# Kernel optimization log

Hardware: AMD Instinct MI355X
Metric: run time of the kernel (lower is better)

The kernel has to match this reference:

```python
import jax, jax.numpy as jnp
import numpy as np

MNIST_IM_SIZE = 784
LATENT = 128
BATCH_SIZE = 8192
ETA = 1.0
GAMMA = 1.0
EPS8 = 1e-8


def setup_inputs() -> dict:
    key = jax.random.key(0)
    ks = jax.random.split(key, 8)
    s = 0.02  # weight init scale
    H = MNIST_IM_SIZE * 4          # 3136
    D2 = MNIST_IM_SIZE // 2        # 392
    return {
        "x": jax.random.uniform(ks[0], (BATCH_SIZE, MNIST_IM_SIZE), jnp.float32),
        "eps": jax.random.normal(ks[1], (BATCH_SIZE, LATENT), jnp.float32),
        "W11": jax.random.normal(ks[2], (MNIST_IM_SIZE, H), jnp.float32) * s,
        "b11": jnp.zeros((H,), jnp.float32),
        "W31": jax.random.normal(ks[3], (H, LATENT), jnp.float32) * s,
        "b31": jnp.zeros((LATENT,), jnp.float32),
        "W32": jax.random.normal(ks[4], (H, LATENT), jnp.float32) * s,
        "b32": jnp.zeros((LATENT,), jnp.float32),
        "W44": jax.random.normal(ks[5], (LATENT, D2), jnp.float32) * s,
        "b44": jnp.zeros((D2,), jnp.float32),
        "W61": jax.random.normal(ks[6], (D2, MNIST_IM_SIZE), jnp.float32) * s,
        "b61": jnp.zeros((MNIST_IM_SIZE,), jnp.float32),
    }


def _clog(t):
    # torch BCELoss clamps log at -100
    return jnp.clip(jnp.log(t), -100.0)


def reference(x, eps, W11, b11, W31, b31, W32, b32, W44, b44, W61, b61):
    b2 = BATCH_SIZE // 2

    def encode(xi):
        enc = jax.nn.relu(xi @ W11 + b11)            # [b2, 4*IM]
        mu = jax.nn.relu(enc @ W31 + b31)            # [b2, LATENT]
        sigma = jax.nn.relu(enc @ W32 + b32)         # [b2, LATENT]
        return mu, sigma

    def decode(z):
        dec = jax.nn.relu(z @ W44 + b44)             # [b2, IM/2]
        dec = jax.nn.relu(dec @ W61 + b61)           # [b2, IM]
        return jax.nn.sigmoid(dec)

    x1, x2 = x[:b2], x[b2:]
    mu1, sig1 = encode(x1)
    mu2, sig2 = encode(x2)
    z1 = eps[:b2] * sig1 + mu1
    z2 = eps[b2:] * sig2 + mu2
    y = jnp.concatenate([decode(z1), decode(z2)], axis=0)  # [B, IM]

    # ---- MAE_loss ----
    sigma1 = sig1 + EPS8
    sigma2 = sig2 + EPS8
    rec_loss = -jnp.sum(x * _clog(y) + (1.0 - x) * _clog(1.0 - y))

    sig_m = (sigma1 + sigma2) * 0.5
    mu_m = (mu1 + mu2) * 0.5
    dkl_pq = 0.5 * jnp.sum(-1.0 - jnp.log(EPS8 + sig_m ** 2) + mu_m ** 2 + sig_m ** 2, axis=1)  # [b2]

    # Covariances are diagonal (as_strided diag copy) -> closed forms:
    # inv_cov = diag(1/sigma); det = prod(sigma); trace(inv_cov2 @ cov1) = sum(sigma1/sigma2)
    det1 = jnp.prod(sigma1, axis=1)                  # [b2]
    det2 = jnp.prod(sigma2, axis=1)                  # [b2]
    trace = jnp.sum(sigma1 / sigma2, axis=1)         # [b2]
    diff = mu2 - mu1
    dquad = jnp.sum(diff * diff / sigma2, axis=1)    # [b2]  (diff^T inv_cov2 diff)
    e = jnp.log(EPS8 + det2 / (det1 + EPS8)) - LATENT  # [b2]

    # torch broadcasting artifact: [b2,1,1]+[b2]+[b2] -> [b2,1,b2] -> resize(b2,b2)
    # => D[i,j] = 0.5*(dquad[i] + trace[j] + e[j])
    D = 0.5 * (dquad[:, None] + trace[None, :] + e[None, :])  # [b2, b2]

    l_diverse = jnp.sum(jnp.log1p(jnp.exp(-D)), axis=1)       # [b2]
    mean_qq = jnp.mean(D, axis=1)                             # [b2]
    # torch (b2,b2) - (b2,) broadcasts mean over the LAST axis (per column)
    l_smooth = jnp.sqrt(jnp.sum((D - mean_qq) ** 2, axis=1) / (LATENT - 1))

    loss = rec_loss + jnp.sum(dkl_pq) + ETA * jnp.sum(l_diverse) + GAMMA * jnp.sum(l_smooth)
    return y, loss
```

## Files before the change

kernel.cpp:

```cpp
#include <hip/hip_runtime.h>
#include <hip/hip_bf16.h>
#include <math.h>

#define BATCH   8192
#define IM      784
#define HDIM    3136
#define LAT     128
#define D2      392
#define B2      4096

#define IM_P    800
#define HDIM_P  3200
#define N2_P    256
#define D2_P    512
#define IM_NP   896
#define KSPLIT  4
#define K2S     (HDIM_P / KSPLIT)
#define REC_BLOCKS ((IM_NP / 128) * (BATCH / 128))

typedef __attribute__((ext_vector_type(8))) short short8;
typedef __attribute__((ext_vector_type(4))) float f32x4;

__device__ __forceinline__ void async_load16(const __hip_bfloat16* g, __hip_bfloat16* l)
{
    __builtin_amdgcn_global_load_lds(
        (const __attribute__((address_space(1))) unsigned int*)g,
        (__attribute__((address_space(3))) unsigned int*)l,
        16, 0, 0);
}

template <int L>
__device__ __forceinline__ void wait_tiles2(int rem)
{
    if (rem >= 2)      asm volatile("s_waitcnt vmcnt(%0)" :: "i"(2 * L) : "memory");
    else if (rem == 1) asm volatile("s_waitcnt vmcnt(%0)" :: "i"(L) : "memory");
    else               asm volatile("s_waitcnt vmcnt(0)" ::: "memory");
}
#define RAW_BARRIER() asm volatile("s_barrier" ::: "memory")

#define PB_X    3200
#define PB_W11  (PB_X   + 2500)
#define PB_W3   (PB_W11 + 800)
#define PB_W44  (PB_W3  + 64)
#define PB_W61  (PB_W44 + 448)
#define PB_END  (PB_W61 + 13)

__device__ __forceinline__ void transpose_tile(
    const float* __restrict__ in, __hip_bfloat16* __restrict__ out,
    int K, int N, int K_pad, int N_pad, int bx, int by, int tid)
{
    __shared__ float tile[32][33];
    int k0 = bx * 32, n0 = by * 32;
    int tx = tid & 31, ty = tid >> 5;
    #pragma unroll
    for (int j = 0; j < 4; ++j) {
        int k = k0 + ty + j * 8, n = n0 + tx;
        tile[ty + j * 8][tx] = (k < K && n < N) ? in[(size_t)k * N + n] : 0.f;
    }
    __syncthreads();
    #pragma unroll
    for (int j = 0; j < 4; ++j) {
        int n = n0 + ty + j * 8, k = k0 + tx;
        if (n < N_pad && k < K_pad)
            out[(size_t)n * K_pad + k] = __float2bfloat16(tile[tx][ty + j * 8]);
    }
}

__global__ __launch_bounds__(256)
void prep(const float* __restrict__ x,
          const float* __restrict__ W11, const float* __restrict__ W31,
          const float* __restrict__ W32, const float* __restrict__ W44,
          const float* __restrict__ W61,
          const float* __restrict__ b11, const float* __restrict__ b31,
          const float* __restrict__ b32, const float* __restrict__ b44,
          const float* __restrict__ b61,
          __hip_bfloat16* __restrict__ x_bf, __hip_bfloat16* __restrict__ W11T,
          __hip_bfloat16* __restrict__ W3xT, __hip_bfloat16* __restrict__ W44T,
          __hip_bfloat16* __restrict__ W61T,
          float* __restrict__ b11p, float* __restrict__ b3x,
          float* __restrict__ b44p, float* __restrict__ b61p)
{
    const int bid = blockIdx.x, tid = threadIdx.x;
    if (bid < PB_X) {
        int gid = bid * 256 + tid;
        int m = gid / 100, ch = gid % 100;
        short8 v = {};
        if (ch < 98) {
            const float* src = x + (size_t)m * IM + ch * 8;
            float4 f0 = *reinterpret_cast<const float4*>(src);
            float4 f1 = *reinterpret_cast<const float4*>(src + 4);
            float f[8] = {f0.x, f0.y, f0.z, f0.w, f1.x, f1.y, f1.z, f1.w};
            #pragma unroll
            for (int k = 0; k < 8; ++k) {
                __hip_bfloat16 h = __float2bfloat16(f[k]);
                v[k] = *reinterpret_cast<short*>(&h);
            }
        }
        *reinterpret_cast<short8*>(&x_bf[(size_t)m * IM_P + ch * 8]) = v;
    } else if (bid < PB_W11) {
        int r = bid - PB_X;
        transpose_tile(W11, W11T, IM, HDIM, IM_P, HDIM_P, r % 25, r / 25, tid);
    } else if (bid < PB_W3) {
        int r = bid - PB_W11;
        int zz = r / 400; r %= 400;
        transpose_tile(zz ? W32 : W31, W3xT + (size_t)zz * 128 * HDIM_P,
                       HDIM, LAT, HDIM_P, 128, r % 100, r / 100, tid);
    } else if (bid < PB_W44) {
        int r = bid - PB_W3;
        transpose_tile(W44, W44T, LAT, D2, LAT, D2_P, r % 4, r / 4, tid);
    } else if (bid < PB_W61) {
        int r = bid - PB_W44;
        transpose_tile(W61, W61T, D2, IM, D2_P, IM_NP, r % 16, r / 16, tid);
    } else {
        int i = (bid - PB_W61) * 256 + tid;
        if (i < HDIM_P) b11p[i] = (i < HDIM) ? b11[i] : 0.f;
        if (i < LAT) { b3x[i] = b31[i]; b3x[LAT + i] = b32[i]; }
        if (i < D2_P) b44p[i] = (i < D2) ? b44[i] : 0.f;
        if (i < IM_NP) b61p[i] = (i < IM) ? b61[i] : 0.f;
    }
}

template <int BN, typename OutT, bool SIGMOID, bool FUSE_REC>
__global__ __launch_bounds__(256)
void gemm_mfma(const __hip_bfloat16* __restrict__ A, const __hip_bfloat16* __restrict__ BT,
               const float* __restrict__ bias, OutT* __restrict__ C,
               int K_pad, int N_logical, int ldc,
               const float* __restrict__ xin, double* __restrict__ rec_arr)
{
    constexpr int NI = BN / 32;
    constexpr int SL = (BN == 128) ? 4 : 3;
    __shared__ alignas(16) __hip_bfloat16 As[3][128 * 32];
    __shared__ alignas(16) __hip_bfloat16 Bs[3][BN * 32];
    __shared__ float shr[4];

    const int t    = threadIdx.x;
    const int wave = t >> 6;
    const int lane = t & 63;
    const int wr   = wave >> 1;
    const int wc   = wave & 1;

    const int nwg = gridDim.x * gridDim.y;
    const int wg  = blockIdx.y * gridDim.x + blockIdx.x;
    const int swz = (wg & 7) * (nwg >> 3) + (wg >> 3);
    const int m0  = (swz / gridDim.x) * 128;
    const int n0  = (swz % gridDim.x) * BN;

    const int srow = lane & 15;
    const int skc  = lane >> 4;
    const __hip_bfloat16* Ag = A + (size_t)(m0 + wave * 32 + srow) * K_pad + skc * 8;
    const __hip_bfloat16* Bg;
    if constexpr (BN == 128)
        Bg = BT + (size_t)(n0 + wave * 32 + srow) * K_pad + skc * 8;
    else
        Bg = BT + (size_t)(n0 + wave * 16 + srow) * K_pad + skc * 8;

    auto stage = [&](int buf, int kt) {
        async_load16(Ag + kt, &As[buf][(wave * 2 + 0) * 512]);
        async_load16(Ag + (size_t)16 * K_pad + kt, &As[buf][(wave * 2 + 1) * 512]);
        if constexpr (BN == 128) {
            async_load16(Bg + kt, &Bs[buf][(wave * 2 + 0) * 512]);
            async_load16(Bg + (size_t)16 * K_pad + kt, &Bs[buf][(wave * 2 + 1) * 512]);
        } else {
            async_load16(Bg + kt, &Bs[buf][wave * 512]);
        }
    };

    f32x4 acc[4][NI] = {};
    const int nt = K_pad >> 5;

    stage(0, 0);
    if (nt > 1) stage(1, 32);

    int cur = 0;
    for (int tt = 0; tt < nt; ++tt) {
        int stg = cur + 2; if (stg >= 3) stg -= 3;
        if (tt + 2 < nt) stage(stg, (tt + 2) << 5);
        wait_tiles2<SL>(nt - 1 - tt);
        __builtin_amdgcn_sched_barrier(0);
        RAW_BARRIER();

        short8 af[4], bfv[NI];
        #pragma unroll
        for (int mi = 0; mi < 4; ++mi)
            af[mi] = *reinterpret_cast<const short8*>(&As[cur][(wr * 4 + mi) * 512 + lane * 8]);
        #pragma unroll
        for (int ni = 0; ni < NI; ++ni)
            bfv[ni] = *reinterpret_cast<const short8*>(&Bs[cur][(wc * NI + ni) * 512 + lane * 8]);

        #pragma unroll
        for (int mi = 0; mi < 4; ++mi)
            #pragma unroll
            for (int ni = 0; ni < NI; ++ni)
                acc[mi][ni] = __builtin_amdgcn_mfma_f32_16x16x32_bf16(
                    af[mi], bfv[ni], acc[mi][ni], 0, 0, 0);

        RAW_BARRIER();
        cur = (cur + 1 == 3) ? 0 : cur + 1;
    }

    const int fr   = lane & 15;
    const int row4 = (lane >> 4) * 4;
    float rsum = 0.f;
    #pragma unroll
    for (int ni = 0; ni < NI; ++ni) {
        int gn = n0 + wc * (BN / 2) + ni * 16 + fr;
        if (gn >= N_logical) continue;
        float bv = bias[gn];
        #pragma unroll
        for (int mi = 0; mi < 4; ++mi) {
            #pragma unroll
            for (int r = 0; r < 4; ++r) {
                int gm = m0 + wr * 64 + mi * 16 + row4 + r;
                float o = acc[mi][ni][r] + bv;
                o = fmaxf(o, 0.f);
                if (SIGMOID) o = 1.f / (1.f + expf(-o));
                if constexpr (sizeof(OutT) == 2)
                    C[(size_t)gm * ldc + gn] = __float2bfloat16(o);
                else
                    C[(size_t)gm * ldc + gn] = o;
                if constexpr (FUSE_REC) {
                    float xv = xin[(size_t)gm * ldc + gn];
                    float l1 = fmaxf(__logf(o), -100.f);
                    float l2 = fmaxf(__logf(1.f - o), -100.f);
                    rsum += xv * l1 + (1.f - xv) * l2;
                }
            }
        }
    }
    if constexpr (FUSE_REC) {
        for (int off = 32; off; off >>= 1) rsum += __shfl_down(rsum, off);
        if (lane == 0) shr[wave] = rsum;
        __syncthreads();
        if (t == 0)
            rec_arr[wg] = (double)(-(shr[0] + shr[1] + shr[2] + shr[3]));
    }
}

__global__ __launch_bounds__(256)
void gemm_mfma_splitk(const __hip_bfloat16* __restrict__ A, const __hip_bfloat16* __restrict__ BT,
                      float* __restrict__ partial, int K_pad)
{
    constexpr int BN = 64, NI = 2, SL = 3;
    __shared__ alignas(16) __hip_bfloat16 As[3][128 * 32];
    __shared__ alignas(16) __hip_bfloat16 Bs[3][BN * 32];

    const int t    = threadIdx.x;
    const int wave = t >> 6;
    const int lane = t & 63;
    const int wr   = wave >> 1;
    const int wc   = wave & 1;

    const int nwg = gridDim.x * gridDim.y;
    const int wg  = blockIdx.y * gridDim.x + blockIdx.x;
    const int swz = (wg & 7) * (nwg >> 3) + (wg >> 3);
    const int m0  = (swz / gridDim.x) * 128;
    const int n0  = (swz % gridDim.x) * BN;
    const int koff = blockIdx.z * K2S;

    const int srow = lane & 15;
    const int skc  = lane >> 4;
    const __hip_bfloat16* Ag = A + (size_t)(m0 + wave * 32 + srow) * K_pad + skc * 8 + koff;
    const __hip_bfloat16* Bg = BT + (size_t)(n0 + wave * 16 + srow) * K_pad + skc * 8 + koff;

    auto stage = [&](int buf, int kt) {
        async_load16(Ag + kt, &As[buf][(wave * 2 + 0) * 512]);
        async_load16(Ag + (size_t)16 * K_pad + kt, &As[buf][(wave * 2 + 1) * 512]);
        async_load16(Bg + kt, &Bs[buf][wave * 512]);
    };

    f32x4 acc[4][NI] = {};
    const int nt = K2S >> 5;

    stage(0, 0);
    stage(1, 32);

    int cur = 0;
    for (int tt = 0; tt < nt; ++tt) {
        int stg = cur + 2; if (stg >= 3) stg -= 3;
        if (tt + 2 < nt) stage(stg, (tt + 2) << 5);
        wait_tiles2<SL>(nt - 1 - tt);
        __builtin_amdgcn_sched_barrier(0);
        RAW_BARRIER();

        short8 af[4], bfv[NI];
        #pragma unroll
        for (int mi = 0; mi < 4; ++mi)
            af[mi] = *reinterpret_cast<const short8*>(&As[cur][(wr * 4 + mi) * 512 + lane * 8]);
        #pragma unroll
        for (int ni = 0; ni < NI; ++ni)
            bfv[ni] = *reinterpret_cast<const short8*>(&Bs[cur][(wc * NI + ni) * 512 + lane * 8]);

        #pragma unroll
        for (int mi = 0; mi < 4; ++mi)
            #pragma unroll
            for (int ni = 0; ni < NI; ++ni)
                acc[mi][ni] = __builtin_amdgcn_mfma_f32_16x16x32_bf16(
                    af[mi], bfv[ni], acc[mi][ni], 0, 0, 0);

        RAW_BARRIER();
        cur = (cur + 1 == 3) ? 0 : cur + 1;
    }

    const int fr   = lane & 15;
    const int row4 = (lane >> 4) * 4;
    float* out = partial + (size_t)blockIdx.z * BATCH * 256;
    #pragma unroll
    for (int ni = 0; ni < NI; ++ni) {
        int gn = n0 + wc * 32 + ni * 16 + fr;
        #pragma unroll
        for (int mi = 0; mi < 4; ++mi) {
            #pragma unroll
            for (int r = 0; r < 4; ++r) {
                int gm = m0 + wr * 64 + mi * 16 + row4 + r;
                out[(size_t)gm * 256 + gn] = acc[mi][ni][r];
            }
        }
    }
}

__global__ __launch_bounds__(128)
void reduce_stats(const float* __restrict__ partial, const float* __restrict__ b3x,
                  const float* __restrict__ eps, __hip_bfloat16* __restrict__ z,
                  float* __restrict__ a_out, float* __restrict__ c_out,
                  float* __restrict__ dkl_out)
{
    const int b = blockIdx.x;
    const int j = threadIdx.x;
    const size_t r1 = (size_t)b * 256;
    const size_t r2 = (size_t)(B2 + b) * 256;

    float mu1 = 0.f, sg1 = 0.f, mu2 = 0.f, sg2 = 0.f;
    #pragma unroll
    for (int s = 0; s < KSPLIT; ++s) {
        const float* p = partial + (size_t)s * BATCH * 256;
        mu1 += p[r1 + j];  sg1 += p[r1 + 128 + j];
        mu2 += p[r2 + j];  sg2 += p[r2 + 128 + j];
    }
    const float bm = b3x[j], bs = b3x[128 + j];
    mu1 = fmaxf(mu1 + bm, 0.f); sg1 = fmaxf(sg1 + bs, 0.f);
    mu2 = fmaxf(mu2 + bm, 0.f); sg2 = fmaxf(sg2 + bs, 0.f);
    z[(size_t)b * LAT + j]        = __float2bfloat16(fmaf(eps[(size_t)b * LAT + j], sg1, mu1));
    z[(size_t)(B2 + b) * LAT + j] = __float2bfloat16(fmaf(eps[(size_t)(B2 + b) * LAT + j], sg2, mu2));

    float s1 = sg1 + 1e-8f, s2 = sg2 + 1e-8f;
    float sm = 0.5f * (s1 + s2), mm = 0.5f * (mu1 + mu2);
    float dkl = -1.f - logf(1e-8f + sm * sm) + mm * mm + sm * sm;
    float tr  = s1 / s2;
    float df  = mu2 - mu1;
    float dq  = df * df / s2;
    float p1  = s1, p2 = s2;

    for (int off = 32; off; off >>= 1) {
        dkl += __shfl_down(dkl, off);
        tr  += __shfl_down(tr, off);
        dq  += __shfl_down(dq, off);
        p1  *= __shfl_down(p1, off);
        p2  *= __shfl_down(p2, off);
    }
    __shared__ float sh[5][2];
    const int wid = j >> 6;
    if ((j & 63) == 0) { sh[0][wid] = dkl; sh[1][wid] = tr; sh[2][wid] = dq;
                         sh[3][wid] = p1;  sh[4][wid] = p2; }
    __syncthreads();
    if (j == 0) {
        dkl = sh[0][0] + sh[0][1];
        tr  = sh[1][0] + sh[1][1];
        dq  = sh[2][0] + sh[2][1];
        p1  = sh[3][0] * sh[3][1];
        p2  = sh[4][0] * sh[4][1];
        float e = logf(1e-8f + p2 / (p1 + 1e-8f)) - (float)LAT;
        a_out[b]   = 0.5f * dq;
        c_out[b]   = 0.5f * (tr + e);
        dkl_out[b] = 0.5f * dkl;
    }
}

__global__ __launch_bounds__(1024)
void moments_kernel(const float* __restrict__ a, const float* __restrict__ c,
                    const float* __restrict__ dkl, double* __restrict__ accs)
{
    __shared__ double sh[4][16];
    const int tid = threadIdx.x, wid = tid >> 6, lane = tid & 63;
    double sd = 0.0, p1 = 0.0, p2 = 0.0, q = 0.0;
    #pragma unroll
    for (int k = 0; k < 4; ++k) {
        int i = tid + k * 1024;
        double av = a[i], cv = c[i];
        sd += dkl[i];
        p1 += cv;
        p2 += av;
        double d = cv - av;
        q  += d * d;
    }
    for (int off = 32; off; off >>= 1) {
        sd += __shfl_down(sd, off);
        p1 += __shfl_down(p1, off);
        p2 += __shfl_down(p2, off);
        q  += __shfl_down(q, off);
    }
    if (lane == 0) { sh[0][wid] = sd; sh[1][wid] = p1; sh[2][wid] = p2; sh[3][wid] = q; }
    __syncthreads();
    if (tid == 0) {
        double SD = 0, P1 = 0, P2 = 0, Q = 0;
        for (int w = 0; w < 16; ++w) { SD += sh[0][w]; P1 += sh[1][w]; P2 += sh[2][w]; Q += sh[3][w]; }
        double cbar = P1 / (double)B2;
        accs[1] = SD;
        accs[4] = -P2;
        accs[5] = Q - 2.0 * cbar * (P1 - P2) + (double)B2 * cbar * cbar;
    }
}

__global__ __launch_bounds__(256)
void ldiv_smooth(const float* __restrict__ a, const float* __restrict__ c,
                 const double* __restrict__ accs,
                 float* __restrict__ ld_out, double* __restrict__ sm_out)
{
    __shared__ float sh[4];
    int i = blockIdx.x;
    float ai = a[i];
    float part = 0.f;
    const float4* c4 = reinterpret_cast<const float4*>(c);
    for (int j4 = threadIdx.x; j4 < B2 / 4; j4 += 256) {
        float4 cc = c4[j4];
        float cv[4] = {cc.x, cc.y, cc.z, cc.w};
        #pragma unroll
        for (int u = 0; u < 4; ++u) {
            float tv = -(ai + cv[u]);
            float r = (tv > 0.f) ? (tv + log1pf(__expf(-tv))) : log1pf(__expf(tv));
            part += r;
        }
    }
    for (int off = 32; off; off >>= 1) part += __shfl_down(part, off);
    int wid = threadIdx.x >> 6;
    if ((threadIdx.x & 63) == 0) sh[wid] = part;
    __syncthreads();
    if (threadIdx.x == 0) {
        ld_out[i] = sh[0] + sh[1] + sh[2] + sh[3];
        double S1 = accs[4], S2 = accs[5];
        double aa = (double)ai;
        double q = ((double)B2 * aa * aa + 2.0 * aa * S1 + S2) / (double)(LAT - 1);
        sm_out[i] = sqrt(fmax(q, 0.0));
    }
}

__global__ __launch_bounds__(1024)
void final_kernel(const double* __restrict__ rec_arr, const float* __restrict__ ld,
                  const double* __restrict__ sm, const double* __restrict__ accs,
                  float* __restrict__ out_loss)
{
    __shared__ double sh[16];
    const int tid = threadIdx.x, wid = tid >> 6, lane = tid & 63;
    double s = 0.0;
    if (tid < REC_BLOCKS) s += rec_arr[tid];
    #pragma unroll
    for (int k = 0; k < 4; ++k) {
        int i = tid + k * 1024;
        s += (double)ld[i] + sm[i];
    }
    for (int off = 32; off; off >>= 1) s += __shfl_down(s, off);
    if (lane == 0) sh[wid] = s;
    __syncthreads();
    if (tid == 0) {
        double tot = accs[1];
        for (int w = 0; w < 16; ++w) tot += sh[w];
        out_loss[0] = (float)tot;
    }
}

extern "C" void kernel_launch(void* const* d_in, const int* in_sizes, int n_in,
                              void* d_out, int out_size, void* d_ws, size_t ws_size,
                              hipStream_t stream)
{
    const float* x   = (const float*)d_in[0];
    const float* eps = (const float*)d_in[1];
    const float* W11 = (const float*)d_in[2];
    const float* b11 = (const float*)d_in[3];
    const float* W31 = (const float*)d_in[4];
    const float* b31 = (const float*)d_in[5];
    const float* W32 = (const float*)d_in[6];
    const float* b32 = (const float*)d_in[7];
    const float* W44 = (const float*)d_in[8];
    const float* b44 = (const float*)d_in[9];
    const float* W61 = (const float*)d_in[10];
    const float* b61 = (const float*)d_in[11];
    float* out = (float*)d_out;

    char* ws = (char*)d_ws;
    size_t off = 0;
    auto alloc = [&](size_t bytes) {
        void* p = ws + off;
        off += (bytes + 255) & ~(size_t)255;
        return p;
    };
    __hip_bfloat16* x_bf    = (__hip_bfloat16*)alloc((size_t)BATCH * IM_P * 2);
    __hip_bfloat16* W11T    = (__hip_bfloat16*)alloc((size_t)HDIM_P * IM_P * 2);
    float*          b11p    = (float*)alloc(HDIM_P * 4);
    __hip_bfloat16* enc     = (__hip_bfloat16*)alloc((size_t)BATCH * HDIM_P * 2);
    __hip_bfloat16* W3xT    = (__hip_bfloat16*)alloc((size_t)N2_P * HDIM_P * 2);
    float*          b3x     = (float*)alloc(N2_P * 4);
    __hip_bfloat16* z_bf    = (__hip_bfloat16*)alloc((size_t)BATCH * LAT * 2);
    __hip_bfloat16* W44T    = (__hip_bfloat16*)alloc((size_t)D2_P * LAT * 2);
    float*          b44p    = (float*)alloc(D2_P * 4);
    __hip_bfloat16* dec     = (__hip_bfloat16*)alloc((size_t)BATCH * D2_P * 2);
    __hip_bfloat16* W61T    = (__hip_bfloat16*)alloc((size_t)IM_NP * D2_P * 2);
    float*          b61p    = (float*)alloc(IM_NP * 4);
    float*          av      = (float*)alloc(B2 * 4);
    float*          cv      = (float*)alloc(B2 * 4);
    float*          dklv    = (float*)alloc(B2 * 4);
    float*          ldv     = (float*)alloc(B2 * 4);
    double*         smv     = (double*)alloc(B2 * 8);
    double*         rec_arr = (double*)alloc(REC_BLOCKS * 8);
    double*         accs    = (double*)alloc(8 * sizeof(double));
    float*          partial = (float*)alloc((size_t)KSPLIT * BATCH * N2_P * 4);

    hipMemsetAsync(accs, 0, 8 * sizeof(double), stream);

    prep<<<PB_END, 256, 0, stream>>>(x, W11, W31, W32, W44, W61,
                                     b11, b31, b32, b44, b61,
                                     x_bf, W11T, W3xT, W44T, W61T,
                                     b11p, b3x, b44p, b61p);

    gemm_mfma<128, __hip_bfloat16, false, false>
        <<<dim3(HDIM_P / 128, BATCH / 128), 256, 0, stream>>>(
        x_bf, W11T, b11p, enc, IM_P, HDIM_P, HDIM_P, nullptr, nullptr);
    gemm_mfma_splitk<<<dim3(N2_P / 64, BATCH / 128, KSPLIT), 256, 0, stream>>>(
        enc, W3xT, partial, HDIM_P);
    reduce_stats<<<B2, 128, 0, stream>>>(partial, b3x, eps, z_bf, av, cv, dklv);
    moments_kernel<<<1, 1024, 0, stream>>>(av, cv, dklv, accs);
    gemm_mfma<128, __hip_bfloat16, false, false>
        <<<dim3(D2_P / 128, BATCH / 128), 256, 0, stream>>>(
        z_bf, W44T, b44p, dec, LAT, D2_P, D2_P, nullptr, nullptr);
    gemm_mfma<128, float, true, true>
        <<<dim3(IM_NP / 128, BATCH / 128), 256, 0, stream>>>(
        dec, W61T, b61p, out, D2_P, IM, IM, x, rec_arr);
    ldiv_smooth<<<B2, 256, 0, stream>>>(av, cv, accs, ldv, smv);
    final_kernel<<<1, 1024, 0, stream>>>(rec_arr, ldv, smv, accs, out + (size_t)BATCH * IM);
}
```

Measured before the change: 336.5 us.

## Use 8-wave 256x128-tile GEMM with workgroup swizzle for the encoder layer

Replaces the first encoder GEMM (x @ W11) with a new 512-thread kernel that computes a 256x128 output tile per workgroup, using 8 waves in a 4x2 layout with 64x64 per wave. It double-buffers LDS with async global-to-LDS loads and remaps workgroup IDs so neighbouring blocks share operand tiles in cache. The goal is more reuse per loaded tile and a better ratio of MFMA work to loads on the largest GEMM. The tradeoff is higher register pressure from 16 accumulators per wave, only two pipeline stages instead of the earlier three or four, and unvectorised bf16 stores in the epilogue. The swizzle relies on the workgroup count being divisible by 8.

```diff
diff --git a/kernel.cpp b/kernel.cpp
--- a/kernel.cpp
+++ b/kernel.cpp
@@ -29,6 +29,12 @@
         16, 0, 0);
 }
 
+template <int L>
+__device__ __forceinline__ void wait_prev(int rem)
+{
+    if (rem >= 1) asm volatile("s_waitcnt vmcnt(%0)" :: "i"(L) : "memory");
+    else          asm volatile("s_waitcnt vmcnt(0)" ::: "memory");
+}
 template <int L>
 __device__ __forceinline__ void wait_tiles2(int rem)
 {
@@ -120,6 +126,85 @@
     }
 }
 
+__global__ __launch_bounds__(512)
+void gemm_mfma_8w(const __hip_bfloat16* __restrict__ A, const __hip_bfloat16* __restrict__ BT,
+                  const float* __restrict__ bias, __hip_bfloat16* __restrict__ C,
+                  int K_pad, int N_dim)
+{
+    __shared__ alignas(16) __hip_bfloat16 As[2][256 * 32];
+    __shared__ alignas(16) __hip_bfloat16 Bs[2][128 * 32];
+
+    const int t    = threadIdx.x;
+    const int wave = t >> 6;
+    const int lane = t & 63;
+    const int wr   = wave >> 1;
+    const int wc   = wave & 1;
+
+    const int nwg = gridDim.x * gridDim.y;
+    const int wg  = blockIdx.y * gridDim.x + blockIdx.x;
+    const int swz = (wg & 7) * (nwg >> 3) + (wg >> 3);
+    const int m0  = (swz / gridDim.x) * 256;
+    const int n0  = (swz % gridDim.x) * 128;
+
+    const int srow = lane & 15;
+    const int skc  = lane >> 4;
+    const __hip_bfloat16* Ag = A + (size_t)(m0 + wave * 32 + srow) * K_pad + skc * 8;
+    const __hip_bfloat16* Bg = BT + (size_t)(n0 + wave * 16 + srow) * K_pad + skc * 8;
+
+    auto stage = [&](int buf, int kt) {
+        async_load16(Ag + kt, &As[buf][(wave * 2 + 0) * 512]);
+        async_load16(Ag + (size_t)16 * K_pad + kt, &As[buf][(wave * 2 + 1) * 512]);
+        async_load16(Bg + kt, &Bs[buf][wave * 512]);
+    };
+
+    f32x4 acc[4][4] = {};
+    const int nt = K_pad >> 5;
+
+    stage(0, 0);
+
+    for (int tt = 0; tt < nt; ++tt) {
+        if (tt + 1 < nt) stage((tt + 1) & 1, (tt + 1) << 5);
+        wait_prev<3>(nt - 1 - tt);
+        __builtin_amdgcn_sched_barrier(0);
+        RAW_BARRIER();
+
+        const int cur = tt & 1;
+        short8 af[4], bfv[4];
+        #pragma unroll
+        for (int mi = 0; mi < 4; ++mi)
+            af[mi] = *reinterpret_cast<const short8*>(&As[cur][(wr * 4 + mi) * 512 + lane * 8]);
+        #pragma unroll
+        for (int ni = 0; ni < 4; ++ni)
+            bfv[ni] = *reinterpret_cast<const short8*>(&Bs[cur][(wc * 4 + ni) * 512 + lane * 8]);
+
+        #pragma unroll
+        for (int mi = 0; mi < 4; ++mi)
+            #pragma unroll
+            for (int ni = 0; ni < 4; ++ni)
+                acc[mi][ni] = __builtin_amdgcn_mfma_f32_16x16x32_bf16(
+                    af[mi], bfv[ni], acc[mi][ni], 0, 0, 0);
+
+        RAW_BARRIER();
+    }
+
+    const int fr   = lane & 15;
+    const int row4 = (lane >> 4) * 4;
+    #pragma unroll
+    for (int ni = 0; ni < 4; ++ni) {
+        int gn = n0 + wc * 64 + ni * 16 + fr;
+        float bv = bias[gn];
+        #pragma unroll
+        for (int mi = 0; mi < 4; ++mi) {
+            #pragma unroll
+            for (int r = 0; r < 4; ++r) {
+                int gm = m0 + wr * 64 + mi * 16 + row4 + r;
+                float o = fmaxf(acc[mi][ni][r] + bv, 0.f);
+                C[(size_t)gm * N_dim + gn] = __float2bfloat16(o);
+            }
+        }
+    }
+}
+
 template <int BN, typename OutT, bool SIGMOID, bool FUSE_REC>
 __global__ __launch_bounds__(256)
 void gemm_mfma(const __hip_bfloat16* __restrict__ A, const __hip_bfloat16* __restrict__ BT,
@@ -520,9 +605,8 @@
                                      x_bf, W11T, W3xT, W44T, W61T,
                                      b11p, b3x, b44p, b61p);
 
-    gemm_mfma<128, __hip_bfloat16, false, false>
-        <<<dim3(HDIM_P / 128, BATCH / 128), 256, 0, stream>>>(
-        x_bf, W11T, b11p, enc, IM_P, HDIM_P, HDIM_P, nullptr, nullptr);
+    gemm_mfma_8w<<<dim3(HDIM_P / 128, BATCH / 256), 512, 0, stream>>>(
+        x_bf, W11T, b11p, enc, IM_P, HDIM_P);
     gemm_mfma_splitk<<<dim3(N2_P / 64, BATCH / 128, KSPLIT), 256, 0, stream>>>(
         enc, W3xT, partial, HDIM_P);
     reduce_stats<<<B2, 128, 0, stream>>>(partial, b3x, eps, z_bf, av, cv, dklv);
```

Result: faster. 317.0 us (-5.8%).
